# Performance work log

Hardware: AMD Instinct MI355X
Metric: run time of the kernel (lower is better)

The kernel has to match this reference:

```python
import jax, jax.numpy as jnp
import numpy as np

N = 20000      # nodes (atoms)
E = 200000     # directed edges
T = 800000     # triplets
H = 128        # hidden_channels
INT = 64       # int_emb_size
BAS = 8        # basis_emb_size
NS = 7         # num_spherical
NR = 6         # num_radial
OUT = 256      # out_emb_channels
NB = 4         # num_blocks
L = 3          # num_output_layers
CUT = 5.0      # cutoff
silu = jax.nn.silu  # 'swish' activation

# Envelope with exponent=5 -> p=6
_P = 6.0
_A = -(_P + 1.0) * (_P + 2.0) / 2.0   # -28
_B = _P * (_P + 2.0)                  # 48
_C = -_P * (_P + 1.0) / 2.0           # -21

def _envelope(d):
    d5 = d ** 5
    return (1.0 / d + _A * d5 + _B * d5 * d + _C * d5 * d * d) * (d < 1.0).astype(d.dtype)

def setup_inputs() -> dict:
    key = jax.random.key(0)
    ks = iter(jax.random.split(key, 64))
    def p(shape, scale=0.05):
        return jax.random.normal(next(ks), shape, dtype=jnp.float32) * scale
    inp = {}
    inp['z'] = jax.random.randint(next(ks), (N,), 0, 95)
    inp['dist'] = jax.random.uniform(next(ks), (E,), minval=0.1, maxval=CUT, dtype=jnp.float32)
    inp['sbf'] = p((T, NS * NR), 1.0)
    inp['i'] = jax.random.randint(next(ks), (E,), 0, N)
    inp['j'] = jax.random.randint(next(ks), (E,), 0, N)
    inp['idx_kj'] = jax.random.randint(next(ks), (T,), 0, E)
    inp['idx_ji'] = jax.random.randint(next(ks), (T,), 0, E)
    # embedding block params
    s3 = float(np.sqrt(3.0))
    inp['emb_table'] = jax.random.uniform(next(ks), (95, H), minval=-s3, maxval=s3, dtype=jnp.float32)
    inp['W_rbf_emb'] = p((NR, H)); inp['b_rbf_emb'] = jnp.zeros((H,), jnp.float32)
    inp['W_emb'] = p((3 * H, H)); inp['b_emb'] = jnp.zeros((H,), jnp.float32)
    inp['freq'] = jnp.arange(1, NR + 1, dtype=jnp.float32) * jnp.pi
    # interaction blocks (stacked over NB)
    inp['Wi_rbf1'] = p((NB, NR, BAS)); inp['Wi_rbf2'] = p((NB, BAS, H))
    inp['Wi_sbf1'] = p((NB, NS * NR, BAS)); inp['Wi_sbf2'] = p((NB, BAS, INT))
    inp['Wi_kj'] = p((NB, H, H)); inp['bi_kj'] = jnp.zeros((NB, H), jnp.float32)
    inp['Wi_ji'] = p((NB, H, H)); inp['bi_ji'] = jnp.zeros((NB, H), jnp.float32)
    inp['Wi_down'] = p((NB, H, INT)); inp['Wi_up'] = p((NB, INT, H))
    inp['Wi_rb_W1'] = p((NB, H, H)); inp['Wi_rb_b1'] = jnp.zeros((NB, H), jnp.float32)
    inp['Wi_rb_W2'] = p((NB, H, H)); inp['Wi_rb_b2'] = jnp.zeros((NB, H), jnp.float32)
    inp['Wi_lin'] = p((NB, H, H)); inp['bi_lin'] = jnp.zeros((NB, H), jnp.float32)
    inp['Wi_ra_W1'] = p((NB, H, H)); inp['Wi_ra_b1'] = jnp.zeros((NB, H), jnp.float32)
    inp['Wi_ra_W2'] = p((NB, H, H)); inp['Wi_ra_b2'] = jnp.zeros((NB, H), jnp.float32)
    # output blocks (stacked over NB+1)
    inp['Wo_rbf'] = p((NB + 1, NR, H)); inp['Wo_up'] = p((NB + 1, H, OUT))
    inp['Wo_linW'] = p((NB + 1, L, OUT, OUT)); inp['Wo_linb'] = jnp.zeros((NB + 1, L, OUT), jnp.float32)
    return inp

def _forward(z, dist, sbf, i, j, idx_kj, idx_ji,
             emb_table, W_rbf_emb, b_rbf_emb, W_emb, b_emb, freq,
             Wi_rbf1, Wi_rbf2, Wi_sbf1, Wi_sbf2, Wi_kj, bi_kj, Wi_ji, bi_ji,
             Wi_down, Wi_up, Wi_rb_W1, Wi_rb_b1, Wi_rb_W2, Wi_rb_b2,
             Wi_lin, bi_lin, Wi_ra_W1, Wi_ra_b1, Wi_ra_W2, Wi_ra_b2,
             Wo_rbf, Wo_up, Wo_linW, Wo_linb):
    num_nodes = z.shape[0]
    num_edges = dist.shape[0]
    # BesselBasisLayer: rbf [E, NR]
    d = dist / CUT
    rbf = _envelope(d)[:, None] * jnp.sin(freq * d[:, None])
    # EmbeddingBlock -> edge features x [E, H]
    h = emb_table[z]
    rbf_h = silu(rbf @ W_rbf_emb + b_rbf_emb)
    x = silu(jnp.concatenate([h[i], h[j], rbf_h], axis=-1) @ W_emb + b_emb)

    def out_block(b, x_e):
        t = (rbf @ Wo_rbf[b]) * x_e                      # [E, H]
        node = jax.ops.segment_sum(t, i, num_segments=num_nodes)
        node = node @ Wo_up[b]                            # [N, OUT]
        for l in range(L):
            node = silu(node @ Wo_linW[b, l] + Wo_linb[b, l])
        return node

    P = out_block(0, x)
    for b in range(NB):
        # InteractionPPBlock
        x_ji = silu(x @ Wi_ji[b] + bi_ji[b])
        x_kj = silu(x @ Wi_kj[b] + bi_kj[b])
        rbf_b = (rbf @ Wi_rbf1[b]) @ Wi_rbf2[b]           # [E, H]
        x_kj = x_kj * rbf_b
        x_kj = silu(x_kj @ Wi_down[b])                    # [E, INT]
        sbf_b = (sbf @ Wi_sbf1[b]) @ Wi_sbf2[b]           # [T, INT]
        x_kj = x_kj[idx_kj] * sbf_b                       # gather triplets
        x_kj = jax.ops.segment_sum(x_kj, idx_ji, num_segments=num_edges)
        x_kj = silu(x_kj @ Wi_up[b])                      # [E, H]
        hdd = x_ji + x_kj
        # one residual layer before skip (num_before_skip=1)
        hdd = hdd + silu(silu(hdd @ Wi_rb_W1[b] + Wi_rb_b1[b]) @ Wi_rb_W2[b] + Wi_rb_b2[b])
        hdd = silu(hdd @ Wi_lin[b] + bi_lin[b]) + x
        # one residual layer after skip (source uses num_before_skip here too)
        hdd = hdd + silu(silu(hdd @ Wi_ra_W1[b] + Wi_ra_b1[b]) @ Wi_ra_W2[b] + Wi_ra_b2[b])
        x = hdd
        P = P + out_block(b + 1, x)
    return P  # [N, OUT] per-node output embeddings

def reference(z, dist, sbf, i, j, idx_kj, idx_ji,
              emb_table, W_rbf_emb, b_rbf_emb, W_emb, b_emb, freq,
              Wi_rbf1, Wi_rbf2, Wi_sbf1, Wi_sbf2, Wi_kj, bi_kj, Wi_ji, bi_ji,
              Wi_down, Wi_up, Wi_rb_W1, Wi_rb_b1, Wi_rb_W2, Wi_rb_b2,
              Wi_lin, bi_lin, Wi_ra_W1, Wi_ra_b1, Wi_ra_W2, Wi_ra_b2,
              Wo_rbf, Wo_up, Wo_linW, Wo_linb):
    return _forward(z, dist, sbf, i, j, idx_kj, idx_ji,
                    emb_table, W_rbf_emb, b_rbf_emb, W_emb, b_emb, freq,
                    Wi_rbf1, Wi_rbf2, Wi_sbf1, Wi_sbf2, Wi_kj, bi_kj, Wi_ji, bi_ji,
                    Wi_down, Wi_up, Wi_rb_W1, Wi_rb_b1, Wi_rb_W2, Wi_rb_b2,
                    Wi_lin, bi_lin, Wi_ra_W1, Wi_ra_b1, Wi_ra_W2, Wi_ra_b2,
                    Wo_rbf, Wo_up, Wo_linW, Wo_linb)
```

## Files before the change

### kernel.cpp

```cpp
#include <hip/hip_runtime.h>
#include <hip/hip_bf16.h>

#define NND 20000
#define NE  200000
#define NT  800000

#define SW256(row) (((row) & 7) << 4)
#define SW128(row) (((row) & 7) << 4)

typedef short  s16x8 __attribute__((ext_vector_type(8)));
typedef float  f32x4 __attribute__((ext_vector_type(4)));

__device__ __forceinline__ float silu_f(float v) {
    return v * __builtin_amdgcn_rcpf(1.0f + __expf(-v));
}

__device__ __forceinline__ ushort f2bf(float f) {
    uint u = __float_as_uint(f);
    uint r = (u + 0x7FFFu + ((u >> 16) & 1u)) >> 16;
    return (ushort)r;
}
__device__ __forceinline__ float bf2f(ushort u) {
    return __uint_as_float(((uint)u) << 16);
}
__device__ __forceinline__ uint f2bf_pk(float a, float b) {
    __hip_bfloat162 h = __float22bfloat162_rn(make_float2(a, b));
    return *(uint*)&h;
}
__device__ __forceinline__ void store_bf4(void* p, float v0, float v1, float v2, float v3) {
    uint2 o;
    o.x = f2bf_pk(v0, v1);
    o.y = f2bf_pk(v2, v3);
    *(uint2*)p = o;
}

__global__ void rbf_kernel(const float* __restrict__ dist, const float* __restrict__ freq,
                           float* __restrict__ rbf, int E)
{
    int e = blockIdx.x * blockDim.x + threadIdx.x;
    if (e >= E) return;
    float d = dist[e] * 0.2f;
    float d5 = d * d; d5 = d5 * d5 * d;
    float env = 1.0f / d + (-28.0f) * d5 + 48.0f * d5 * d + (-21.0f) * d5 * d * d;
    env = (d < 1.0f) ? env : 0.0f;
    float fr[6];
    #pragma unroll
    for (int r = 0; r < 6; ++r) fr[r] = freq[r];
    #pragma unroll
    for (int r = 0; r < 6; ++r)
        rbf[(size_t)e * 6 + r] = env * sinf(fr[r] * d);
}

__global__ void twt_kernel(const float* __restrict__ W, ushort* __restrict__ Wt,
                           int CIN, int COUT, int total)
{
    int idx = blockIdx.x * 256 + threadIdx.x;
    if (idx >= total) return;
    int per = CIN * COUT;
    int b = idx / per, r = idx % per;
    int k = r / COUT, c = r % COUT;
    Wt[(size_t)b * per + (size_t)c * CIN + k] = f2bf(W[idx]);
}

__global__ void twt7_kernel(const float* __restrict__ s0, const float* __restrict__ s1,
                            const float* __restrict__ s2, const float* __restrict__ s3,
                            const float* __restrict__ s4, const float* __restrict__ s5,
                            const float* __restrict__ s6, ushort* __restrict__ dst)
{
    int idx = blockIdx.x * 256 + threadIdx.x;
    int which = idx >> 16;
    int r = idx & 65535;
    const float* s = (which == 0) ? s0 : (which == 1) ? s1 : (which == 2) ? s2 :
                     (which == 3) ? s3 : (which == 4) ? s4 : (which == 5) ? s5 : s6;
    int b = r >> 14;
    int rr = r & 16383;
    int k = rr >> 7, c = rr & 127;
    dst[(size_t)which * 65536 + b * 16384 + c * 128 + k] = f2bf(s[r]);
}

template<int CIN, int COUT, int MODE, typename IT, typename ET, typename OT>
__global__ __launch_bounds__(256) void mfma_lin_kernel(
    const IT* __restrict__ x, const ushort* __restrict__ Wt,
    const float* __restrict__ bias, const ET* __restrict__ extra,
    OT* __restrict__ y, int M)
{
    constexpr int MT = 64;
    constexpr int NF = COUT / 16;
    constexpr int KS = CIN / 32;
    constexpr int PITCH = CIN * 2;
    __shared__ ushort As_u[MT * CIN];
    __shared__ ushort Ws_u[COUT * CIN];
    char* As = (char*)As_u;
    char* Ws = (char*)Ws_u;
    const int tid = threadIdx.x;
    const int row0 = blockIdx.x * MT;
    const bool full = (row0 + MT <= M);

    constexpr int ACH = MT * CIN / 8;
    for (int c = tid; c < ACH; c += 256) {
        int row = c / (CIN / 8);
        int kc  = c % (CIN / 8);
        int grow = row0 + row;
        s16x8 v;
        if (full || grow < M) {
            if constexpr (sizeof(IT) == 4) {
                const float* src = (const float*)x + (size_t)grow * CIN + kc * 8;
                float4 f0 = *(const float4*)(src);
                float4 f1 = *(const float4*)(src + 4);
                v[0] = (short)f2bf(f0.x); v[1] = (short)f2bf(f0.y);
                v[2] = (short)f2bf(f0.z); v[3] = (short)f2bf(f0.w);
                v[4] = (short)f2bf(f1.x); v[5] = (short)f2bf(f1.y);
                v[6] = (short)f2bf(f1.z); v[7] = (short)f2bf(f1.w);
            } else {
                v = *(const s16x8*)((const ushort*)x + (size_t)grow * CIN + kc * 8);
            }
        } else {
            #pragma unroll
            for (int u = 0; u < 8; ++u) v[u] = 0;
        }
        *(s16x8*)(As + ((row * PITCH + kc * 16) ^ SW256(row))) = v;
    }
    constexpr int WCH = COUT * CIN / 8;
    for (int c = tid; c < WCH; c += 256) {
        int col = c / (CIN / 8);
        int kc  = c % (CIN / 8);
        s16x8 v = *(const s16x8*)(Wt + (size_t)col * CIN + kc * 8);
        *(s16x8*)(Ws + ((col * PITCH + kc * 16) ^ SW256(col))) = v;
    }
    __syncthreads();

    const int w = tid >> 6, lane = tid & 63;
    const int l15 = lane & 15, l4 = lane >> 4;
    const int arow = w * 16 + l15;

    f32x4 acc[NF];
    #pragma unroll
    for (int nf = 0; nf < NF; ++nf) acc[nf] = (f32x4){0.f, 0.f, 0.f, 0.f};

    #pragma unroll
    for (int ks = 0; ks < KS; ++ks) {
        const int kbyte = (ks * 32 + l4 * 8) * 2;
        s16x8 a = *(const s16x8*)(As + ((arow * PITCH + kbyte) ^ SW256(arow)));
        #pragma unroll
        for (int nf = 0; nf < NF; ++nf) {
            int col = nf * 16 + l15;
            s16x8 bf = *(const s16x8*)(Ws + ((col * PITCH + kbyte) ^ SW256(col)));
            acc[nf] = __builtin_amdgcn_mfma_f32_16x16x32_bf16(bf, a, acc[nf], 0, 0, 0);
        }
    }

    const int grow = row0 + w * 16 + l15;
    if (grow < M) {
        #pragma unroll
        for (int nf = 0; nf < NF; ++nf) {
            int c0 = nf * 16 + l4 * 4;
            float4 bv = make_float4(0.f, 0.f, 0.f, 0.f);
            if (bias) bv = *(const float4*)(bias + c0);
            float v0 = acc[nf][0] + bv.x, v1 = acc[nf][1] + bv.y;
            float v2 = acc[nf][2] + bv.z, v3 = acc[nf][3] + bv.w;
            if constexpr (MODE & 1) {
                v0 = silu_f(v0); v1 = silu_f(v1); v2 = silu_f(v2); v3 = silu_f(v3);
            }
            if constexpr ((MODE & 4) != 0) {
                if constexpr (sizeof(ET) == 4) {
                    float4 ex = *(const float4*)((const float*)extra + (size_t)grow * COUT + c0);
                    v0 += ex.x; v1 += ex.y; v2 += ex.z; v3 += ex.w;
                } else {
                    ushort4 ex = *(const ushort4*)((const ushort*)extra + (size_t)grow * COUT + c0);
                    v0 += bf2f(ex.x); v1 += bf2f(ex.y); v2 += bf2f(ex.z); v3 += bf2f(ex.w);
                }
            }
            if constexpr (sizeof(OT) == 4) {
                float* o = (float*)y + (size_t)grow * COUT + c0;
                if constexpr (MODE & 8) {
                    float4 cur = *(const float4*)o;
                    v0 += cur.x; v1 += cur.y; v2 += cur.z; v3 += cur.w;
                }
                *(float4*)o = make_float4(v0, v1, v2, v3);
            } else {
                store_bf4((ushort*)y + (size_t)grow * COUT + c0, v0, v1, v2, v3);
            }
        }
    }
}

__global__ __launch_bounds__(256) void mfma_front_kernel(
    const ushort* __restrict__ x,
    const ushort* __restrict__ Wt1, const ushort* __restrict__ Wt2,
    const ushort* __restrict__ Wtd,
    const float* __restrict__ b1, const float* __restrict__ b2,
    const float* __restrict__ rbf, const float* __restrict__ W1r,
    const float* __restrict__ W2r,
    ushort* __restrict__ y1, ushort* __restrict__ yd, int M)
{
    constexpr int PITCH = 256;
    __shared__ ushort A_u[64 * 128];
    __shared__ ushort W1_u[128 * 128];
    __shared__ ushort W2_u[128 * 128];
    char* A = (char*)A_u;
    char* W1s = (char*)W1_u;
    char* W2s = (char*)W2_u;
    const int tid = threadIdx.x;
    const int row0 = blockIdx.x * 64;

    for (int c = tid; c < 1024; c += 256) {
        int row = c >> 4, kc = c & 15;
        s16x8 v = *(const s16x8*)(x + (size_t)(row0 + row) * 128 + kc * 8);
        *(s16x8*)(A + ((row * PITCH + kc * 16) ^ SW256(row))) = v;
    }
    for (int c = tid; c < 2048; c += 256) {
        int col = c >> 4, kc = c & 15;
        int o = (col * PITCH + kc * 16) ^ SW256(col);
        *(s16x8*)(W1s + o) = *(const s16x8*)(Wt1 + (size_t)col * 128 + kc * 8);
        *(s16x8*)(W2s + o) = *(const s16x8*)(Wt2 + (size_t)col * 128 + kc * 8);
    }
    s16x8 wdreg[4];
    #pragma unroll
    for (int i = 0; i < 4; ++i) {
        int c = tid + i * 256;
        wdreg[i] = *(const s16x8*)(Wtd + (size_t)(c >> 4) * 128 + (c & 15) * 8);
    }
    __syncthreads();

    const int w = tid >> 6, lane = tid & 63;
    const int l15 = lane & 15, l4 = lane >> 4;
    const int arow = w * 16 + l15;

    f32x4 acc1[8], acc2[8];
    #pragma unroll
    for (int nf = 0; nf < 8; ++nf) {
        acc1[nf] = (f32x4){0.f, 0.f, 0.f, 0.f};
        acc2[nf] = (f32x4){0.f, 0.f, 0.f, 0.f};
    }
    #pragma unroll
    for (int ks = 0; ks < 4; ++ks) {
        const int kbyte = (ks * 32 + l4 * 8) * 2;
        s16x8 a = *(const s16x8*)(A + ((arow * PITCH + kbyte) ^ SW256(arow)));
        #pragma unroll
        for (int nf = 0; nf < 8; ++nf) {
            int col = nf * 16 + l15;
            int o = (col * PITCH + kbyte) ^ SW256(col);
            s16x8 bf1 = *(const s16x8*)(W1s + o);
            s16x8 bf2 = *(const s16x8*)(W2s + o);
            acc1[nf] = __builtin_amdgcn_mfma_f32_16x16x32_bf16(bf1, a, acc1[nf], 0, 0, 0);
            acc2[nf] = __builtin_amdgcn_mfma_f32_16x16x32_bf16(bf2, a, acc2[nf], 0, 0, 0);
        }
    }
    __syncthreads();

    const int grow = row0 + arow;
    float rv[6];
    #pragma unroll
    for (int q = 0; q < 6; ++q) rv[q] = rbf[(size_t)grow * 6 + q];
    float t8[8];
    #pragma unroll
    for (int p = 0; p < 8; ++p) {
        float s = 0.f;
        #pragma unroll
        for (int q = 0; q < 6; ++q) s += rv[q] * W1r[q * 8 + p];
        t8[p] = s;
    }
    #pragma unroll
    for (int nf = 0; nf < 8; ++nf) {
        int c0 = nf * 16 + l4 * 4;
        float4 bb1 = *(const float4*)(b1 + c0);
        float4 bb2 = *(const float4*)(b2 + c0);
        store_bf4(y1 + (size_t)grow * 128 + c0,
                  silu_f(acc1[nf][0] + bb1.x), silu_f(acc1[nf][1] + bb1.y),
                  silu_f(acc1[nf][2] + bb1.z), silu_f(acc1[nf][3] + bb1.w));
        float r0 = 0.f, r1 = 0.f, r2 = 0.f, r3 = 0.f;
        #pragma unroll
        for (int p = 0; p < 8; ++p) {
            float4 wq = *(const float4*)(W2r + p * 128 + c0);
            float tp = t8[p];
            r0 += tp * wq.x; r1 += tp * wq.y; r2 += tp * wq.z; r3 += tp * wq.w;
        }
        store_bf4(A + ((arow * PITCH + c0 * 2) ^ SW256(arow)),
                  silu_f(acc2[nf][0] + bb2.x) * r0, silu_f(acc2[nf][1] + bb2.y) * r1,
                  silu_f(acc2[nf][2] + bb2.z) * r2, silu_f(acc2[nf][3] + bb2.w) * r3);
    }
    #pragma unroll
    for (int i = 0; i < 4; ++i) {
        int c = tid + i * 256;
        int col = c >> 4, kc = c & 15;
        *(s16x8*)(W1s + ((col * PITCH + kc * 16) ^ SW256(col))) = wdreg[i];
    }
    __syncthreads();

    f32x4 accd[4];
    #pragma unroll
    for (int nf = 0; nf < 4; ++nf) accd[nf] = (f32x4){0.f, 0.f, 0.f, 0.f};
    #pragma unroll
    for (int ks = 0; ks < 4; ++ks) {
        const int kbyte = (ks * 32 + l4 * 8) * 2;
        s16x8 a = *(const s16x8*)(A + ((arow * PITCH + kbyte) ^ SW256(arow)));
        #pragma unroll
        for (int nf = 0; nf < 4; ++nf) {
            int col = nf * 16 + l15;
            s16x8 bf = *(const s16x8*)(W1s + ((col * PITCH + kbyte) ^ SW256(col)));
            accd[nf] = __builtin_amdgcn_mfma_f32_16x16x32_bf16(bf, a, accd[nf], 0, 0, 0);
        }
    }
    #pragma unroll
    for (int nf = 0; nf < 4; ++nf) {
        int c0 = nf * 16 + l4 * 4;
        store_bf4(yd + (size_t)grow * 64 + c0,
                  silu_f(accd[nf][0]), silu_f(accd[nf][1]),
                  silu_f(accd[nf][2]), silu_f(accd[nf][3]));
    }
}

__global__ __launch_bounds__(256) void mfma_back_kernel(
    const ushort* __restrict__ go, const ushort* __restrict__ xji,
    const ushort* __restrict__ x,
    const ushort* __restrict__ Wup, const ushort* __restrict__ Wrb1,
    const ushort* __restrict__ Wrb2, const ushort* __restrict__ Wlin,
    const ushort* __restrict__ Wra1, const ushort* __restrict__ Wra2,
    const float* __restrict__ b_rb1, const float* __restrict__ b_rb2,
    const float* __restrict__ b_lin, const float* __restrict__ b_ra1,
    const float* __restrict__ b_ra2,
    ushort* __restrict__ xout, int M)
{
    __shared__ ushort A_u[64 * 128];
    __shared__ ushort T_u[64 * 128];
    char* A  = (char*)A_u;
    char* Tb = (char*)T_u;
    const int tid = threadIdx.x;
    const int row0 = blockIdx.x * 64;
    const int w = tid >> 6, lane = tid & 63;
    const int l15 = lane & 15, l4 = lane >> 4;
    const int colbase = w * 32;

    f32x4 acc[8];
    s16x8 wfA[8], wfB[8];
    ushort4 xr[8];

    auto zero_acc = [&]() {
        #pragma unroll
        for (int i = 0; i < 8; ++i) acc[i] = (f32x4){0.f, 0.f, 0.f, 0.f};
    };
    auto load_w8 = [&](s16x8* wf, const ushort* Wg) {
        #pragma unroll
        for (int nfi = 0; nfi < 2; ++nfi)
            #pragma unroll
            for (int ks = 0; ks < 4; ++ks)
                wf[nfi * 4 + ks] = *(const s16x8*)(
                    Wg + (size_t)(colbase + nfi * 16 + l15) * 128 + ks * 32 + l4 * 8);
    };
    auto load_rows = [&](const ushort* src) {
        #pragma unroll
        for (int rt = 0; rt < 4; ++rt) {
            int grow = row0 + rt * 16 + l15;
            #pragma unroll
            for (int nfi = 0; nfi < 2; ++nfi) {
                int c0 = colbase + nfi * 16 + l4 * 4;
                xr[rt * 2 + nfi] = *(const ushort4*)(src + (size_t)grow * 128 + c0);
            }
        }
    };
    auto run_phase = [&](char* Ab, const s16x8* wf) {
        #pragma unroll
        for (int rt = 0; rt < 4; ++rt) {
            int row = rt * 16 + l15;
            #pragma unroll
            for (int ks = 0; ks < 4; ++ks) {
                s16x8 a = *(const s16x8*)(Ab + ((row * 256 + ks * 64 + l4 * 16) ^ SW256(row)));
                acc[rt * 2 + 0] = __builtin_amdgcn_mfma_f32_16x16x32_bf16(wf[0 * 4 + ks], a, acc[rt * 2 + 0], 0, 0, 0);
                acc[rt * 2 + 1] = __builtin_amdgcn_mfma_f32_16x16x32_bf16(wf[1 * 4 + ks], a, acc[rt * 2 + 1], 0, 0, 0);
            }
        }
    };

    s16x8 wfUp[4];
    #pragma unroll
    for (int nfi = 0; nfi < 2; ++nfi)
        #pragma unroll
        for (int ks = 0; ks < 2; ++ks)
            wfUp[nfi * 2 + ks] = *(const s16x8*)(
                Wup + (size_t)(colbase + nfi * 16 + l15) * 64 + ks * 32 + l4 * 8);
    for (int c = tid; c < 512; c += 256) {
        int row = c >> 3, kc = c & 7;
        s16x8 v = *(const s16x8*)(go + (size_t)(row0 + row) * 64 + kc * 8);
        *(s16x8*)(Tb + ((row * 128 + kc * 16) ^ SW128(row))) = v;
    }
    load_w8(wfA, Wrb1);
    load_rows(xji);
    __syncthreads();

    zero_acc();
    #pragma unroll
    for (int rt = 0; rt < 4; ++rt) {
        int row = rt * 16 + l15;
        #pragma unroll
        for (int ks = 0; ks < 2; ++ks) {
            s16x8 a = *(const s16x8*)(Tb + ((row * 128 + ks * 64 + l4 * 16) ^ SW128(row)));
            acc[rt * 2 + 0] = __builtin_amdgcn_mfma_f32_16x16x32_bf16(wfUp[0 * 2 + ks], a, acc[rt * 2 + 0], 0, 0, 0);
            acc[rt * 2 + 1] = __builtin_amdgcn_mfma_f32_16x16x32_bf16(wfUp[1 * 2 + ks], a, acc[rt * 2 + 1], 0, 0, 0);
        }
    }
    #pragma unroll
    for (int rt = 0; rt < 4; ++rt) {
        int row = rt * 16 + l15;
        #pragma unroll
        for (int nfi = 0; nfi < 2; ++nfi) {
            int c0 = colbase + nfi * 16 + l4 * 4;
            f32x4 v = acc[rt * 2 + nfi];
            ushort4 xj = xr[rt * 2 + nfi];
            store_bf4(A + ((row * 256 + c0 * 2) ^ SW256(row)),
                      bf2f(xj.x) + silu_f(v[0]), bf2f(xj.y) + silu_f(v[1]),
                      bf2f(xj.z) + silu_f(v[2]), bf2f(xj.w) + silu_f(v[3]));
        }
    }
    __syncthreads();

    load_w8(wfB, Wrb2);
    zero_acc();
    run_phase(A, wfA);
    #pragma unroll
    for (int rt = 0; rt < 4; ++rt) {
        int row = rt * 16 + l15;
        #pragma unroll
        for (int nfi = 0; nfi < 2; ++nfi) {
            int c0 = colbase + nfi * 16 + l4 * 4;
            f32x4 v = acc[rt * 2 + nfi];
            float4 bb = *(const float4*)(b_rb1 + c0);
            store_bf4(Tb + ((row * 256 + c0 * 2) ^ SW256(row)),
                      silu_f(v[0] + bb.x), silu_f(v[1] + bb.y),
                      silu_f(v[2] + bb.z), silu_f(v[3] + bb.w));
        }
    }
    __syncthreads();

    load_w8(wfA, Wlin);
    load_rows(x);
    zero_acc();
    run_phase(Tb, wfB);
    #pragma unroll
    for (int rt = 0; rt < 4; ++rt) {
        int row = rt * 16 + l15;
        #pragma unroll
        for (int nfi = 0; nfi < 2; ++nfi) {
            int c0 = colbase + nfi * 16 + l4 * 4;
            f32x4 v = acc[rt * 2 + nfi];
            float4 bb = *(const float4*)(b_rb2 + c0);
            int ao = (row * 256 + c0 * 2) ^ SW256(row);
            ushort4 h = *(const ushort4*)(A + ao);
            store_bf4(A + ao,
                      bf2f(h.x) + silu_f(v[0] + bb.x), bf2f(h.y) + silu_f(v[1] + bb.y),
                      bf2f(h.z) + silu_f(v[2] + bb.z), bf2f(h.w) + silu_f(v[3] + bb.w));
        }
    }
    __syncthreads();

    load_w8(wfB, Wra1);
    zero_acc();
    run_phase(A, wfA);
    __syncthreads();
    #pragma unroll
    for (int rt = 0; rt < 4; ++rt) {
        int row = rt * 16 + l15;
        #pragma unroll
        for (int nfi = 0; nfi < 2; ++nfi) {
            int c0 = colbase + nfi * 16 + l4 * 4;
            f32x4 v = acc[rt * 2 + nfi];
            float4 bb = *(const float4*)(b_lin + c0);
            ushort4 xv = xr[rt * 2 + nfi];
            store_bf4(A + ((row * 256 + c0 * 2) ^ SW256(row)),
                      silu_f(v[0] + bb.x) + bf2f(xv.x), silu_f(v[1] + bb.y) + bf2f(xv.y),
                      silu_f(v[2] + bb.z) + bf2f(xv.z), silu_f(v[3] + bb.w) + bf2f(xv.w));
        }
    }
    __syncthreads();

    load_w8(wfA, Wra2);
    zero_acc();
    run_phase(A, wfB);
    #pragma unroll
    for (int rt = 0; rt < 4; ++rt) {
        int row = rt * 16 + l15;
        #pragma unroll
        for (int nfi = 0; nfi < 2; ++nfi) {
            int c0 = colbase + nfi * 16 + l4 * 4;
            f32x4 v = acc[rt * 2 + nfi];
            float4 bb = *(const float4*)(b_ra1 + c0);
            store_bf4(Tb + ((row * 256 + c0 * 2) ^ SW256(row)),
                      silu_f(v[0] + bb.x), silu_f(v[1] + bb.y),
                      silu_f(v[2] + bb.z), silu_f(v[3] + bb.w));
        }
    }
    __syncthreads();

    zero_acc();
    run_phase(Tb, wfA);
    #pragma unroll
    for (int rt = 0; rt < 4; ++rt) {
        int row = rt * 16 + l15;
        int grow = row0 + row;
        #pragma unroll
        for (int nfi = 0; nfi < 2; ++nfi) {
            int c0 = colbase + nfi * 16 + l4 * 4;
            f32x4 v = acc[rt * 2 + nfi];
            float4 bb = *(const float4*)(b_ra2 + c0);
            ushort4 h = *(const ushort4*)(A + ((row * 256 + c0 * 2) ^ SW256(row)));
            store_bf4(xout + (size_t)grow * 128 + c0,
                      bf2f(h.x) + silu_f(v[0] + bb.x), bf2f(h.y) + silu_f(v[1] + bb.y),
                      bf2f(h.z) + silu_f(v[2] + bb.z), bf2f(h.w) + silu_f(v[3] + bb.w));
        }
    }
}

__global__ __launch_bounds__(256) void node_gather_kernel(
    const float* __restrict__ rbf, const float* __restrict__ Wo,
    const ushort* __restrict__ x, const int* __restrict__ noffs,
    const int* __restrict__ nedge, ushort* __restrict__ node, int N)
{
    const int tid = threadIdx.x;
    const int col = tid & 127;
    const int n = blockIdx.x * 2 + (tid >> 7);
    if (n >= N) return;
    float wo[6];
    #pragma unroll
    for (int q = 0; q < 6; ++q) wo[q] = Wo[q * 128 + col];
    float acc = 0.f;
    const int k0 = noffs[n], k1 = noffs[n + 1];
    for (int k = k0; k < k1; ++k) {
        int e = nedge[k];
        const float* rb = rbf + (size_t)e * 6;
        float t = wo[0] * rb[0] + wo[1] * rb[1] + wo[2] * rb[2]
                + wo[3] * rb[3] + wo[4] * rb[4] + wo[5] * rb[5];
        acc += t * bf2f(x[(size_t)e * 128 + col]);
    }
    node[(size_t)n * 128 + col] = f2bf(acc);
}

__global__ __launch_bounds__(256) void mfma_out_kernel(
    const ushort* __restrict__ node,
    const ushort* __restrict__ Wup, const ushort* __restrict__ Wlin,
    const float* __restrict__ BL, float* __restrict__ P, int N)
{
    __shared__ ushort A_u[64 * 256];
    __shared__ ushort T_u[64 * 256];
    __shared__ ushort W_u[128 * 128];
    char* A  = (char*)A_u;
    char* Tb = (char*)T_u;
    char* Ws = (char*)W_u;
    const int tid = threadIdx.x;
    const int row0 = blockIdx.x * 64;
    const int w = tid >> 6, lane = tid & 63;
    const int l15 = lane & 15, l4 = lane >> 4;
    const int arow = w * 16 + l15;
    const int grow = row0 + arow;
    const int c_base = l4 * 4;

    f32x4 acc[16];
    s16x8 wreg[8];

    auto prefetch_w = [&](const ushort* base, int stride) {
        #pragma unroll
        for (int i = 0; i < 8; ++i) {
            int c = tid + i * 256;
            int col = c >> 4, kc = c & 15;
            wreg[i] = *(const s16x8*)(base + (size_t)col * stride + kc * 8);
        }
    };
    auto commit_w = [&]() {
        #pragma unroll
        for (int i = 0; i < 8; ++i) {
            int c = tid + i * 256;
            int col = c >> 4, kc = c & 15;
            *(s16x8*)(Ws + ((col * 256 + kc * 16) ^ SW256(col))) = wreg[i];
        }
    };
    auto run8 = [&](char* Ab, int apitch, int kboff, int accoff) {
        #pragma unroll
        for (int ks = 0; ks < 4; ++ks) {
            const int kbw = ks * 64 + l4 * 16;
            s16x8 a = *(const s16x8*)(Ab + ((arow * apitch + kboff + kbw) ^ SW256(arow)));
            #pragma unroll
            for (int nf = 0; nf < 8; ++nf) {
                int col = nf * 16 + l15;
                s16x8 bf = *(const s16x8*)(Ws + ((col * 256 + kbw) ^ SW256(col)));
                acc[accoff + nf] = __builtin_amdgcn_mfma_f32_16x16x32_bf16(bf, a, acc[accoff + nf], 0, 0, 0);
            }
        }
    };

    #pragma unroll
    for (int i = 0; i < 16; ++i) acc[i] = (f32x4){0.f, 0.f, 0.f, 0.f};

    for (int c = tid; c < 1024; c += 256) {
        int row = c >> 4, kc = c & 15;
        int gr = row0 + row;
        s16x8 v;
        if (gr < N) {
            v = *(const s16x8*)(node + (size_t)gr * 128 + kc * 8);
        } else {
            #pragma unroll
            for (int u = 0; u < 8; ++u) v[u] = 0;
        }
        *(s16x8*)(Tb + ((row * 256 + kc * 16) ^ SW256(row))) = v;
    }
    prefetch_w(Wup, 128);
    __syncthreads();
    commit_w();
    prefetch_w(Wup + 128 * 128, 128);
    __syncthreads();
    run8(Tb, 256, 0, 0);
    __syncthreads();
    commit_w();
    prefetch_w(Wlin, 256);
    __syncthreads();
    run8(Tb, 256, 0, 8);
    #pragma unroll
    for (int nf = 0; nf < 16; ++nf) {
        int c0 = nf * 16 + c_base;
        store_bf4(A + ((arow * 512 + c0 * 2) ^ SW256(arow)),
                  acc[nf][0], acc[nf][1], acc[nf][2], acc[nf][3]);
    }
    __syncthreads();

    char* S = A; char* D = Tb;
    for (int l = 0; l < 3; ++l) {
        #pragma unroll
        for (int i = 0; i < 16; ++i) acc[i] = (f32x4){0.f, 0.f, 0.f, 0.f};
        const ushort* WL = Wlin + (size_t)l * 65536;
        for (int q = 0; q < 4; ++q) {
            int ch = q & 1, kh = q >> 1;
            commit_w();
            if (q < 3) {
                int nq = q + 1;
                prefetch_w(WL + (size_t)(nq & 1) * 128 * 256 + (nq >> 1) * 128, 256);
            } else if (l < 2) {
                prefetch_w(Wlin + (size_t)(l + 1) * 65536, 256);
            }
            __syncthreads();
            run8(S, 512, kh * 256, ch * 8);
            __syncthreads();
        }
        const float* bl = BL + l * 256;
        if (l < 2) {
            #pragma unroll
            for (int nf = 0; nf < 16; ++nf) {
                int c0 = nf * 16 + c_base;
                float4 bb = *(const float4*)(bl + c0);
                store_bf4(D + ((arow * 512 + c0 * 2) ^ SW256(arow)),
                          silu_f(acc[nf][0] + bb.x), silu_f(acc[nf][1] + bb.y),
                          silu_f(acc[nf][2] + bb.z), silu_f(acc[nf][3] + bb.w));
            }
            __syncthreads();
            char* tmp = S; S = D; D = tmp;
        } else if (grow < N) {
            #pragma unroll
            for (int nf = 0; nf < 16; ++nf) {
                int c0 = nf * 16 + c_base;
                float4 bb = *(const float4*)(bl + c0);
                float* o = P + (size_t)grow * 256 + c0;
                float4 cur = *(const float4*)o;
                *(float4*)o = make_float4(cur.x + silu_f(acc[nf][0] + bb.x),
                                          cur.y + silu_f(acc[nf][1] + bb.y),
                                          cur.z + silu_f(acc[nf][2] + bb.z),
                                          cur.w + silu_f(acc[nf][3] + bb.w));
            }
        }
    }
}

template<int CIN, int COUT, int MODE, typename OT>
__global__ __launch_bounds__(256) void lin_kernel(
    const float* __restrict__ x, const float* __restrict__ W,
    const float* __restrict__ bias, const float* __restrict__ extra,
    OT* __restrict__ y, int M)
{
    constexpr int MT = 64;
    constexpr int CG = COUT / 4;
    constexpr int RG = 256 / CG;
    constexpr int MR = MT / RG;
    __shared__ float xs[MT * CIN];

    const int row0 = blockIdx.x * MT;
    const int tid  = threadIdx.x;
    const int rem  = M - row0;

    if (rem >= MT) {
        const float4* src = (const float4*)(x + (size_t)row0 * CIN);
        constexpr int TOT4 = (MT * CIN) / 4;
        for (int idx = tid; idx < TOT4; idx += 256)
            ((float4*)xs)[idx] = src[idx];
    } else {
        for (int idx = tid; idx < MT * CIN; idx += 256) {
            int r = idx / CIN;
            xs[idx] = (r < rem) ? x[(size_t)(row0 + r) * CIN + (idx % CIN)] : 0.0f;
        }
    }
    __syncthreads();

    const int cg = tid % CG, rg = tid / CG;
    const int c0 = cg * 4;
    float acc[MR][4];
    #pragma unroll
    for (int m = 0; m < MR; ++m) { acc[m][0]=0; acc[m][1]=0; acc[m][2]=0; acc[m][3]=0; }

    for (int k = 0; k < CIN; ++k) {
        float4 w = *(const float4*)(W + (size_t)k * COUT + c0);
        #pragma unroll
        for (int m = 0; m < MR; ++m) {
            float xv = xs[(rg * MR + m) * CIN + k];
            acc[m][0] += xv * w.x; acc[m][1] += xv * w.y;
            acc[m][2] += xv * w.z; acc[m][3] += xv * w.w;
        }
    }

    float4 bv = make_float4(0.f, 0.f, 0.f, 0.f);
    if (bias) bv = *(const float4*)(bias + c0);

    #pragma unroll
    for (int m = 0; m < MR; ++m) {
        int row = row0 + rg * MR + m;
        if (row >= M) continue;
        float v[4] = { acc[m][0] + bv.x, acc[m][1] + bv.y, acc[m][2] + bv.z, acc[m][3] + bv.w };
        if constexpr (MODE & 1) {
            #pragma unroll
            for (int u = 0; u < 4; ++u) v[u] = silu_f(v[u]);
        }
        if constexpr (sizeof(OT) == 4) {
            *(float4*)((float*)y + (size_t)row * COUT + c0) = make_float4(v[0], v[1], v[2], v[3]);
        } else {
            store_bf4((ushort*)y + (size_t)row * COUT + c0, v[0], v[1], v[2], v[3]);
        }
    }
}

__global__ __launch_bounds__(256) void fuse_embed_kernel(
    const int* __restrict__ z, const int* __restrict__ ii, const int* __restrict__ jj,
    const float* __restrict__ pt1, const float* __restrict__ pt2,
    const ushort* __restrict__ t3, const float* __restrict__ bias,
    ushort* __restrict__ x, int E)
{
    int idx = blockIdx.x * 256 + threadIdx.x;
    int e = idx >> 5;
    if (e >= E) return;
    int c4 = (idx & 31) * 4;
    int zi = z[ii[e]], zj = z[jj[e]];
    float4 a = *(const float4*)(pt1 + zi * 128 + c4);
    float4 b = *(const float4*)(pt2 + zj * 128 + c4);
    ushort4 t = *(const ushort4*)(t3 + (size_t)e * 128 + c4);
    float4 bb = *(const float4*)(bias + c4);
    store_bf4(x + (size_t)e * 128 + c4,
              silu_f(a.x + b.x + bf2f(t.x) + bb.x), silu_f(a.y + b.y + bf2f(t.y) + bb.y),
              silu_f(a.z + b.z + bf2f(t.z) + bb.z), silu_f(a.w + b.w + bf2f(t.w) + bb.w));
}

__global__ __launch_bounds__(256) void s1all_kernel(
    const float* __restrict__ sbf, const float* __restrict__ W1,
    const int* __restrict__ pos, ushort* __restrict__ s1all, int T)
{
    constexpr int TT = 32;
    constexpr int FL = TT * 42;
    __shared__ float s_flat[FL];
    __shared__ float s_w1[4 * 42 * 8];
    __shared__ ushort s_out[TT][4][8];
    const int t0 = blockIdx.x * TT;
    const int tid = threadIdx.x;

    for (int k = tid; k < 4 * 42 * 8; k += 256) s_w1[k] = W1[k];
    if (t0 + TT <= T) {
        const float4* src = (const float4*)(sbf + (size_t)t0 * 42);
        for (int k = tid; k < FL / 4; k += 256)
            ((float4*)s_flat)[k] = src[k];
    } else {
        const size_t base = (size_t)t0 * 42;
        const size_t tot = (size_t)T * 42;
        for (int k = tid; k < FL; k += 256)
            s_flat[k] = (base + k < tot) ? sbf[base + k] : 0.0f;
    }
    __syncthreads();
    {
        int t = tid >> 3, p = tid & 7;
        const float* row = s_flat + t * 42;
        float a0 = 0.f, a1 = 0.f, a2 = 0.f, a3 = 0.f;
        #pragma unroll
        for (int q = 0; q < 42; ++q) {
            float xv = row[q];
            a0 += xv * s_w1[0 * 336 + q * 8 + p];
            a1 += xv * s_w1[1 * 336 + q * 8 + p];
            a2 += xv * s_w1[2 * 336 + q * 8 + p];
            a3 += xv * s_w1[3 * 336 + q * 8 + p];
        }
        s_out[t][0][p] = f2bf(a0);
        s_out[t][1][p] = f2bf(a1);
        s_out[t][2][p] = f2bf(a2);
        s_out[t][3][p] = f2bf(a3);
    }
    __syncthreads();
    if (tid < 128) {
        int t = tid >> 2, b = tid & 3;
        int gt = t0 + t;
        if (gt < T)
            *(s16x8*)(s1all + ((size_t)pos[gt] * 4 + b) * 8) = *(const s16x8*)s_out[t][b];
    }
}

__global__ void count_kernel(const int* __restrict__ seg, int* __restrict__ deg, int T)
{
    int t = blockIdx.x * blockDim.x + threadIdx.x;
    if (t < T) atomicAdd(&deg[seg[t]], 1);
}

__global__ __launch_bounds__(256) void scan1_kernel(const int* __restrict__ deg,
                                                    int* __restrict__ offs,
                                                    int* __restrict__ bsum, int E)
{
    __shared__ int s[256];
    int tid = threadIdx.x;
    int g = blockIdx.x * 256 + tid;
    int v = (g < E) ? deg[g] : 0;
    s[tid] = v;
    __syncthreads();
    for (int d = 1; d < 256; d <<= 1) {
        int t = (tid >= d) ? s[tid - d] : 0;
        __syncthreads();
        s[tid] += t;
        __syncthreads();
    }
    if (g < E) offs[g] = s[tid] - v;
    if (tid == 255) bsum[blockIdx.x] = s[255];
}

__global__ __launch_bounds__(1024) void scan2_kernel(int* __restrict__ bsum, int NB)
{
    __shared__ int s[1024];
    int tid = threadIdx.x;
    int v = (tid < NB) ? bsum[tid] : 0;
    s[tid] = v;
    __syncthreads();
    for (int d = 1; d < 1024; d <<= 1) {
        int t = (tid >= d) ? s[tid - d] : 0;
        __syncthreads();
        s[tid] += t;
        __syncthreads();
    }
    if (tid < NB) bsum[tid] = s[tid] - v;
}

__global__ __launch_bounds__(256) void scan3_kernel(int* __restrict__ offs,
                                                    const int* __restrict__ bsum,
                                                    int E, int T)
{
    int g = blockIdx.x * 256 + threadIdx.x;
    if (g < E) offs[g] += bsum[blockIdx.x];
    if (g == 0) offs[E] = T;
}

__global__ void fill_kernel(const int* __restrict__ idx_ji, const int* __restrict__ idx_kj,
                            const int* __restrict__ offs, int* __restrict__ cursor,
                            int* __restrict__ kj_csr, int* __restrict__ pos, int T)
{
    int t = blockIdx.x * blockDim.x + threadIdx.x;
    if (t >= T) return;
    int ji = idx_ji[t];
    int slot = atomicAdd(&cursor[ji], 1);
    int k = offs[ji] + slot;
    kj_csr[k] = idx_kj[t];
    pos[t] = k;
}

__global__ void fillN_kernel(const int* __restrict__ ii, const int* __restrict__ offs,
                             int* __restrict__ cursor, int* __restrict__ elist, int E)
{
    int e = blockIdx.x * blockDim.x + threadIdx.x;
    if (e >= E) return;
    int n = ii[e];
    int slot = atomicAdd(&cursor[n], 1);
    elist[offs[n] + slot] = e;
}

__global__ __launch_bounds__(256) void gather2_kernel(
    const ushort* __restrict__ s1, const float* __restrict__ W2,
    const ushort* __restrict__ xd, const int* __restrict__ kj_csr,
    const int* __restrict__ offs, ushort* __restrict__ out, int E, int boff)
{
    const int lane = threadIdx.x & 63;
    const int e = blockIdx.x * 4 + (threadIdx.x >> 6);
    if (e >= E) return;
    float w2[8];
    #pragma unroll
    for (int p = 0; p < 8; ++p) w2[p] = W2[p * 64 + lane];
    float accA = 0.0f, accB = 0.0f;
    const int k0 = offs[e], k1 = offs[e + 1];
    int k = k0;
    for (; k + 1 < k1; k += 2) {
        s16x8 sv0 = *(const s16x8*)(s1 + (size_t)k * 32 + boff);
        s16x8 sv1 = *(const s16x8*)(s1 + (size_t)(k + 1) * 32 + boff);
        int kj0 = kj_csr[k];
        int kj1 = kj_csr[k + 1];
        float x0 = bf2f(xd[(size_t)kj0 * 64 + lane]);
        float x1 = bf2f(xd[(size_t)kj1 * 64 + lane]);
        float sb0 = bf2f((ushort)sv0[0]) * w2[0] + bf2f((ushort)sv0[1]) * w2[1]
                  + bf2f((ushort)sv0[2]) * w2[2] + bf2f((ushort)sv0[3]) * w2[3]
                  + bf2f((ushort)sv0[4]) * w2[4] + bf2f((ushort)sv0[5]) * w2[5]
                  + bf2f((ushort)sv0[6]) * w2[6] + bf2f((ushort)sv0[7]) * w2[7];
        float sb1 = bf2f((ushort)sv1[0]) * w2[0] + bf2f((ushort)sv1[1]) * w2[1]
                  + bf2f((ushort)sv1[2]) * w2[2] + bf2f((ushort)sv1[3]) * w2[3]
                  + bf2f((ushort)sv1[4]) * w2[4] + bf2f((ushort)sv1[5]) * w2[5]
                  + bf2f((ushort)sv1[6]) * w2[6] + bf2f((ushort)sv1[7]) * w2[7];
        accA += sb0 * x0;
        accB += sb1 * x1;
    }
    if (k < k1) {
        s16x8 sv = *(const s16x8*)(s1 + (size_t)k * 32 + boff);
        int kj = kj_csr[k];
        float sb = bf2f((ushort)sv[0]) * w2[0] + bf2f((ushort)sv[1]) * w2[1]
                 + bf2f((ushort)sv[2]) * w2[2] + bf2f((ushort)sv[3]) * w2[3]
                 + bf2f((ushort)sv[4]) * w2[4] + bf2f((ushort)sv[5]) * w2[5]
                 + bf2f((ushort)sv[6]) * w2[6] + bf2f((ushort)sv[7]) * w2[7];
        accA += sb * bf2f(xd[(size_t)kj * 64 + lane]);
    }
    out[(size_t)e * 64 + lane] = f2bf(accA + accB);
}

extern "C" void kernel_launch(void* const* d_in, const int* in_sizes, int n_in,
                              void* d_out, int out_size, void* d_ws, size_t ws_size,
                              hipStream_t stream)
{
    const int*   z         = (const int*)  d_in[0];
    const float* dist      = (const float*)d_in[1];
    const float* sbf       = (const float*)d_in[2];
    const int*   ii        = (const int*)  d_in[3];
    const int*   jj        = (const int*)  d_in[4];
    const int*   idx_kj    = (const int*)  d_in[5];
    const int*   idx_ji    = (const int*)  d_in[6];
    const float* emb_table = (const float*)d_in[7];
    const float* W_rbf_emb = (const float*)d_in[8];
    const float* b_rbf_emb = (const float*)d_in[9];
    const float* W_emb     = (const float*)d_in[10];
    const float* b_emb     = (const float*)d_in[11];
    const float* freq      = (const float*)d_in[12];
    const float* Wi_rbf1   = (const float*)d_in[13];
    const float* Wi_rbf2   = (const float*)d_in[14];
    const float* Wi_sbf1   = (const float*)d_in[15];
    const float* Wi_sbf2   = (const float*)d_in[16];
    const float* Wi_kj     = (const float*)d_in[17];
    const float* bi_kj     = (const float*)d_in[18];
    const float* Wi_ji     = (const float*)d_in[19];
    const float* bi_ji     = (const float*)d_in[20];
    const float* Wi_down   = (const float*)d_in[21];
    const float* Wi_up     = (const float*)d_in[22];
    const float* Wi_rb_W1  = (const float*)d_in[23];
    const float* Wi_rb_b1  = (const float*)d_in[24];
    const float* Wi_rb_W2  = (const float*)d_in[25];
    const float* Wi_rb_b2  = (const float*)d_in[26];
    const float* Wi_lin    = (const float*)d_in[27];
    const float* bi_lin    = (const float*)d_in[28];
    const float* Wi_ra_W1  = (const float*)d_in[29];
    const float* Wi_ra_b1  = (const float*)d_in[30];
    const float* Wi_ra_W2  = (const float*)d_in[31];
    const float* Wi_ra_b2  = (const float*)d_in[32];
    const float* Wo_rbf    = (const float*)d_in[33];
    const float* Wo_up     = (const float*)d_in[34];
    const float* Wo_linW   = (const float*)d_in[35];
    const float* Wo_linb   = (const float*)d_in[36];

    const int N = NND, E = NE, T = NT;
    float* ws = (float*)d_ws;
    size_t off = 0;
    float* rbf  = ws + off; off += (size_t)E * 6;
    float* buf0 = ws + off; off += (size_t)E * 128;
    float* buf1 = ws + off; off += (size_t)E * 128;
    float* buf2 = ws + off; off += (size_t)E * 128;
    float* buf3 = ws + off; off += (size_t)E * 64;
    float* buf4 = ws + off; off += (size_t)E * 64;
    int* ideg  = (int*)(ws + off); off += E;
    int* ioffs = (int*)(ws + off); off += E + 1;
    int* icur  = (int*)(ws + off); off += E;
    int* ikj   = (int*)(ws + off); off += T;
    int* ipos  = (int*)(ws + off); off += T;
    int* ibsum = (int*)(ws + off); off += 1024;
    int* ndeg  = (int*)(ws + off); off += N;
    int* noffs = (int*)(ws + off); off += N + 1;
    int* ncur  = (int*)(ws + off); off += N;
    int* nedge = (int*)(ws + off); off += E;
    int* nbsum = (int*)(ws + off); off += 1024;
    float* pt1 = ws + off; off += 95 * 128;
    float* pt2 = ws + off; off += 95 * 128;
    ushort* wt_ji   = (ushort*)(ws + off);
    ushort* wt_kj   = wt_ji   + 4 * 16384;
    ushort* wt_rb1  = wt_kj   + 4 * 16384;
    ushort* wt_rb2  = wt_rb1  + 4 * 16384;
    ushort* wt_lin  = wt_rb2  + 4 * 16384;
    ushort* wt_ra1  = wt_lin  + 4 * 16384;
    ushort* wt_ra2  = wt_ra1  + 4 * 16384;
    ushort* wt_down = wt_ra2  + 4 * 16384;
    ushort* wt_up   = wt_down + 4 * 8192;
    ushort* wt_emb3 = wt_up   + 4 * 8192;
    ushort* wt_oup  = wt_emb3 + 16384;
    ushort* wt_olin = wt_oup  + 5 * 32768;
    off += (7 * 4 * 16384 + 2 * 4 * 8192 + 16384 + 5 * 32768 + 15 * 65536 + 1) / 2;

    ushort* xb     = (ushort*)buf0;
    ushort* xjib   = (ushort*)buf1;
    ushort* rbfhb  = (ushort*)buf2;
    ushort* t3b    = (ushort*)buf1;
    ushort* s1all  = (ushort*)buf2;
    ushort* xdb    = (ushort*)buf3;
    ushort* gob    = (ushort*)buf4;
    ushort* nodeb  = (ushort*)buf3;
    float* P = (float*)d_out;

    const int gridE  = (E + 63) / 64;
    const int gridN  = (N + 63) / 64;
    const int NB_SCAN  = (E + 255) / 256;
    const int NB_SCANN = (N + 255) / 256;

    hipMemsetAsync(d_out, 0, (size_t)N * 256 * 4, stream);

    twt7_kernel<<<7 * 65536 / 256, 256, 0, stream>>>(
        Wi_ji, Wi_kj, Wi_rb_W1, Wi_rb_W2, Wi_lin, Wi_ra_W1, Wi_ra_W2, wt_ji);
    twt_kernel<<<128, 256, 0, stream>>>(Wi_down,  wt_down, 128,  64, 4 * 8192);
    twt_kernel<<<128, 256, 0, stream>>>(Wi_up,    wt_up,    64, 128, 4 * 8192);
    twt_kernel<<<64,  256, 0, stream>>>(W_emb + 256 * 128, wt_emb3, 128, 128, 16384);
    twt_kernel<<<640, 256, 0, stream>>>(Wo_up,   wt_oup,  128, 256, 5 * 32768);
    twt_kernel<<<3840, 256, 0, stream>>>(Wo_linW, wt_olin, 256, 256, 15 * 65536);

    hipMemsetAsync(ideg, 0, (size_t)E * 4, stream);
    count_kernel<<<(T + 255) / 256, 256, 0, stream>>>(idx_ji, ideg, T);
    scan1_kernel<<<NB_SCAN, 256, 0, stream>>>(ideg, ioffs, ibsum, E);
    scan2_kernel<<<1, 1024, 0, stream>>>(ibsum, NB_SCAN);
    scan3_kernel<<<NB_SCAN, 256, 0, stream>>>(ioffs, ibsum, E, T);
    hipMemsetAsync(icur, 0, (size_t)E * 4, stream);
    fill_kernel<<<(T + 255) / 256, 256, 0, stream>>>(idx_ji, idx_kj, ioffs, icur, ikj, ipos, T);

    hipMemsetAsync(ndeg, 0, (size_t)N * 4, stream);
    count_kernel<<<(E + 255) / 256, 256, 0, stream>>>(ii, ndeg, E);
    scan1_kernel<<<NB_SCANN, 256, 0, stream>>>(ndeg, noffs, nbsum, N);
    scan2_kernel<<<1, 1024, 0, stream>>>(nbsum, NB_SCANN);
    scan3_kernel<<<NB_SCANN, 256, 0, stream>>>(noffs, nbsum, N, E);
    hipMemsetAsync(ncur, 0, (size_t)N * 4, stream);
    fillN_kernel<<<(E + 255) / 256, 256, 0, stream>>>(ii, noffs, ncur, nedge, E);

    rbf_kernel<<<(E + 255) / 256, 256, 0, stream>>>(dist, freq, rbf, E);
    lin_kernel<6, 128, 1, ushort><<<gridE, 256, 0, stream>>>(rbf, W_rbf_emb, b_rbf_emb, nullptr, rbfhb, E);
    lin_kernel<128, 128, 0, float><<<2, 256, 0, stream>>>(emb_table, W_emb, nullptr, nullptr, pt1, 95);
    lin_kernel<128, 128, 0, float><<<2, 256, 0, stream>>>(emb_table, W_emb + 128 * 128, nullptr, nullptr, pt2, 95);
    mfma_lin_kernel<128, 128, 0, ushort, float, ushort><<<gridE, 256, 0, stream>>>(
        rbfhb, wt_emb3, nullptr, nullptr, t3b, E);
    fuse_embed_kernel<<<(E * 32 + 255) / 256, 256, 0, stream>>>(z, ii, jj, pt1, pt2, t3b, b_emb, xb, E);
    s1all_kernel<<<(T + 31) / 32, 256, 0, stream>>>(sbf, Wi_sbf1, ipos, s1all, T);

    auto out_block = [&](int b) {
        node_gather_kernel<<<(N + 1) / 2, 256, 0, stream>>>(
            rbf, Wo_rbf + (size_t)b * 6 * 128, xb, noffs, nedge, nodeb, N);
        mfma_out_kernel<<<gridN, 256, 0, stream>>>(
            nodeb, wt_oup + (size_t)b * 32768, wt_olin + (size_t)b * 3 * 65536,
            Wo_linb + (size_t)b * 3 * 256, P, N);
    };

    out_block(0);

    for (int b = 0; b < 4; ++b) {
        mfma_front_kernel<<<gridE, 256, 0, stream>>>(
            xb, wt_ji + (size_t)b * 16384, wt_kj + (size_t)b * 16384,
            wt_down + (size_t)b * 8192,
            bi_ji + b * 128, bi_kj + b * 128,
            rbf, Wi_rbf1 + (size_t)b * 48, Wi_rbf2 + (size_t)b * 1024,
            xjib, xdb, E);
        gather2_kernel<<<(E + 3) / 4, 256, 0, stream>>>(
            s1all, Wi_sbf2 + (size_t)b * 512, xdb, ikj, ioffs, gob, E, b * 8);
        mfma_back_kernel<<<gridE, 256, 0, stream>>>(
            gob, xjib, xb,
            wt_up + (size_t)b * 8192, wt_rb1 + (size_t)b * 16384,
            wt_rb2 + (size_t)b * 16384, wt_lin + (size_t)b * 16384,
            wt_ra1 + (size_t)b * 16384, wt_ra2 + (size_t)b * 16384,
            Wi_rb_b1 + b * 128, Wi_rb_b2 + b * 128, bi_lin + b * 128,
            Wi_ra_b1 + b * 128, Wi_ra_b2 + b * 128,
            xb, E);

        out_block(b + 1);
    }
}
```

Measured before the change: 1.922 ms.

## Merge output-block node gather into triplet gather kernel via block-range split

The per-block node gather for the output block is folded into the triplet gather kernel: extra blocks beyond the edge range run the node aggregation on the same x. The output MLP for block b then runs after the back kernel, and a separate node buffer is allocated so it no longer aliases xd. This removes one launch per interaction block and lets the two independent gathers share the GPU instead of running back to back. In exchange the output-block schedule is reordered and more workspace is used.

```diff
diff --git a/kernel.cpp b/kernel.cpp
--- a/kernel.cpp
+++ b/kernel.cpp
@@ -874,13 +874,37 @@
     elist[offs[n] + slot] = e;
 }
 
-__global__ __launch_bounds__(256) void gather2_kernel(
+__global__ __launch_bounds__(256) void gather_ng_kernel(
     const ushort* __restrict__ s1, const float* __restrict__ W2,
     const ushort* __restrict__ xd, const int* __restrict__ kj_csr,
-    const int* __restrict__ offs, ushort* __restrict__ out, int E, int boff)
-{
+    const int* __restrict__ offs, ushort* __restrict__ out, int E, int boff,
+    const float* __restrict__ rbf, const float* __restrict__ Wo,
+    const ushort* __restrict__ x, const int* __restrict__ noffs,
+    const int* __restrict__ nedge, ushort* __restrict__ node, int N, int gridG)
+{
+    const int bid = blockIdx.x;
+    if (bid >= gridG) {
+        const int tid = threadIdx.x;
+        const int col = tid & 127;
+        const int n = (bid - gridG) * 2 + (tid >> 7);
+        if (n >= N) return;
+        float wo[6];
+        #pragma unroll
+        for (int q = 0; q < 6; ++q) wo[q] = Wo[q * 128 + col];
+        float acc = 0.f;
+        const int k0 = noffs[n], k1 = noffs[n + 1];
+        for (int k = k0; k < k1; ++k) {
+            int e = nedge[k];
+            const float* rb = rbf + (size_t)e * 6;
+            float t = wo[0] * rb[0] + wo[1] * rb[1] + wo[2] * rb[2]
+                    + wo[3] * rb[3] + wo[4] * rb[4] + wo[5] * rb[5];
+            acc += t * bf2f(x[(size_t)e * 128 + col]);
+        }
+        node[(size_t)n * 128 + col] = f2bf(acc);
+        return;
+    }
     const int lane = threadIdx.x & 63;
-    const int e = blockIdx.x * 4 + (threadIdx.x >> 6);
+    const int e = bid * 4 + (threadIdx.x >> 6);
     if (e >= E) return;
     float w2[8];
     #pragma unroll
@@ -969,6 +993,7 @@
     float* buf2 = ws + off; off += (size_t)E * 128;
     float* buf3 = ws + off; off += (size_t)E * 64;
     float* buf4 = ws + off; off += (size_t)E * 64;
+    float* buf5 = ws + off; off += (size_t)N * 64;
     int* ideg  = (int*)(ws + off); off += E;
     int* ioffs = (int*)(ws + off); off += E + 1;
     int* icur  = (int*)(ws + off); off += E;
@@ -1003,11 +1028,13 @@
     ushort* s1all  = (ushort*)buf2;
     ushort* xdb    = (ushort*)buf3;
     ushort* gob    = (ushort*)buf4;
-    ushort* nodeb  = (ushort*)buf3;
+    ushort* nodeb  = (ushort*)buf5;
     float* P = (float*)d_out;
 
     const int gridE  = (E + 63) / 64;
     const int gridN  = (N + 63) / 64;
+    const int gridG  = (E + 3) / 4;
+    const int ngBlk  = (N + 1) / 2;
     const int NB_SCAN  = (E + 255) / 256;
     const int NB_SCANN = (N + 255) / 256;
 
@@ -1046,16 +1073,6 @@
     fuse_embed_kernel<<<(E * 32 + 255) / 256, 256, 0, stream>>>(z, ii, jj, pt1, pt2, t3b, b_emb, xb, E);
     s1all_kernel<<<(T + 31) / 32, 256, 0, stream>>>(sbf, Wi_sbf1, ipos, s1all, T);
 
-    auto out_block = [&](int b) {
-        node_gather_kernel<<<(N + 1) / 2, 256, 0, stream>>>(
-            rbf, Wo_rbf + (size_t)b * 6 * 128, xb, noffs, nedge, nodeb, N);
-        mfma_out_kernel<<<gridN, 256, 0, stream>>>(
-            nodeb, wt_oup + (size_t)b * 32768, wt_olin + (size_t)b * 3 * 65536,
-            Wo_linb + (size_t)b * 3 * 256, P, N);
-    };
-
-    out_block(0);
-
     for (int b = 0; b < 4; ++b) {
         mfma_front_kernel<<<gridE, 256, 0, stream>>>(
             xb, wt_ji + (size_t)b * 16384, wt_kj + (size_t)b * 16384,
@@ -1063,8 +1080,9 @@
             bi_ji + b * 128, bi_kj + b * 128,
             rbf, Wi_rbf1 + (size_t)b * 48, Wi_rbf2 + (size_t)b * 1024,
             xjib, xdb, E);
-        gather2_kernel<<<(E + 3) / 4, 256, 0, stream>>>(
-            s1all, Wi_sbf2 + (size_t)b * 512, xdb, ikj, ioffs, gob, E, b * 8);
+        gather_ng_kernel<<<gridG + ngBlk, 256, 0, stream>>>(
+            s1all, Wi_sbf2 + (size_t)b * 512, xdb, ikj, ioffs, gob, E, b * 8,
+            rbf, Wo_rbf + (size_t)b * 6 * 128, xb, noffs, nedge, nodeb, N, gridG);
         mfma_back_kernel<<<gridE, 256, 0, stream>>>(
             gob, xjib, xb,
             wt_up + (size_t)b * 8192, wt_rb1 + (size_t)b * 16384,
@@ -1073,7 +1091,13 @@
             Wi_rb_b1 + b * 128, Wi_rb_b2 + b * 128, bi_lin + b * 128,
             Wi_ra_b1 + b * 128, Wi_ra_b2 + b * 128,
             xb, E);
-
-        out_block(b + 1);
-    }
-}
+        mfma_out_kernel<<<gridN, 256, 0, stream>>>(
+            nodeb, wt_oup + (size_t)b * 32768, wt_olin + (size_t)b * 3 * 65536,
+            Wo_linb + (size_t)b * 3 * 256, P, N);
+    }
+    node_gather_kernel<<<ngBlk, 256, 0, stream>>>(
+        rbf, Wo_rbf + (size_t)4 * 6 * 128, xb, noffs, nedge, nodeb, N);
+    mfma_out_kernel<<<gridN, 256, 0, stream>>>(
+        nodeb, wt_oup + (size_t)4 * 32768, wt_olin + (size_t)4 * 3 * 65536,
+        Wo_linb + (size_t)4 * 3 * 256, P, N);
+}
```

Measured after the change: 1.925 ms. About the same (+0.2%).
